# Optimization experiments

Hardware: AMD Instinct MI355X
Metric: run time of the kernel (lower is better)

The kernel has to match this reference:

```python
import jax, jax.numpy as jnp
import numpy as np

B, N, D, V, K = 64, 256, 512, 50257, 100
NORM_TERM = float(np.log(V))        # norm_term='auto' -> log(vocab)
BACKOFF_PROB = 1e-10


def setup_inputs() -> dict:
    key = jax.random.key(0)
    k1, k2, k3, k4, k5 = jax.random.split(key, 5)
    inp = jax.random.normal(k1, (B, N, D), jnp.float32)
    emb_weight = jax.random.normal(k2, (V, D), jnp.float32) * 0.02
    emb_bias = jnp.zeros((V,), jnp.float32)
    # noise distribution buffer: probs clamped + renormed, then log (as in __init__)
    freqs = jax.random.uniform(k3, (V,), jnp.float32, 1e-3, 1.0)
    probs = freqs / freqs.sum()
    probs = jnp.clip(probs, BACKOFF_PROB)
    logprob_noise = jnp.log(probs / probs.sum())
    target = jax.random.randint(k4, (B, N), 0, V)
    # alias.draw(1,1,K).expand(B,N,K): a single shared set of K noise samples
    noise_samples = jax.random.randint(k5, (K,), 0, V)
    return {
        "input": inp,
        "emb_weight": emb_weight,
        "emb_bias": emb_bias,
        "logprob_noise": logprob_noise,
        "target": target,
        "noise_samples": noise_samples,
    }


def reference(input, emb_weight, emb_bias, logprob_noise, target, noise_samples):
    k = noise_samples.shape[0]
    # logits under the noise distribution (pure gathers)
    logit_target_in_noise = logprob_noise[target]          # (B, N)
    logit_noise_in_noise = logprob_noise[noise_samples]    # (K,)
    # model scores: gathered embedding rows dotted with hidden states
    tgt_emb = emb_weight[target]                           # (B, N, D)
    logit_target_in_model = (
        jnp.einsum("bnd,bnd->bn", input, tgt_emb) + emb_bias[target] - NORM_TERM
    )                                                      # (B, N)
    noise_emb = emb_weight[noise_samples]                  # (K, D)
    logit_noise_in_model = (
        jnp.einsum("bnd,kd->bnk", input, noise_emb)
        + emb_bias[noise_samples][None, None, :]
        - NORM_TERM
    )                                                      # (B, N, K)
    # NCE: p_true = exp(lm) / (exp(lm) + K*exp(ln)) = sigmoid(lm - ln - log K)
    # BCE with label [1, 0, ..., 0]:
    #   -loss = log_sigmoid(x) at target slot, log_sigmoid(-x) at noise slots
    log_k = jnp.log(jnp.asarray(k, dtype=input.dtype))
    x_t = logit_target_in_model - logit_target_in_noise - log_k             # (B, N)
    x_n = logit_noise_in_model - logit_noise_in_noise[None, None, :] - log_k  # (B, N, K)
    per_pos = jax.nn.log_sigmoid(x_t) + jnp.sum(jax.nn.log_sigmoid(-x_n), axis=2)
    return jnp.sum(per_pos, axis=1)  # (B,)
```

## Files before the change

kernel.cpp:

```cpp
#include <hip/hip_runtime.h>
#include <math.h>

#define Dq 512
#define Vq 50257
#define Kq 100
#define KP 112
#define NORM_TERM 10.8249051f
#define LOGK 4.6051702f
#define NBLK 512
#define DT_STRIDE 3584

typedef __attribute__((ext_vector_type(8))) short short8;
typedef __attribute__((ext_vector_type(4))) float floatx4;
typedef __attribute__((ext_vector_type(4))) unsigned short ushort4v;
typedef __attribute__((ext_vector_type(8))) unsigned short ushort8v;

__device__ __forceinline__ unsigned short f2bf(float f) {
    union { float f; unsigned u; } v; v.f = f;
    unsigned r = v.u + 0x7FFFu + ((v.u >> 16) & 1u);
    return (unsigned short)(r >> 16);
}

__device__ __forceinline__ short8 cvt8(floatx4 a, floatx4 b) {
    short8 o;
    o[0] = (short)f2bf(a.x); o[1] = (short)f2bf(a.y);
    o[2] = (short)f2bf(a.z); o[3] = (short)f2bf(a.w);
    o[4] = (short)f2bf(b.x); o[5] = (short)f2bf(b.y);
    o[6] = (short)f2bf(b.z); o[7] = (short)f2bf(b.w);
    return o;
}

__device__ __forceinline__ float dot4(floatx4 a, floatx4 b) {
    return a.x*b.x + a.y*b.y + a.z*b.z + a.w*b.w;
}

__device__ __forceinline__ float log_sigmoid(float x) {
    return fminf(x, 0.f) - __logf(1.f + __expf(-fabsf(x)));
}

__global__ void prep_noise(const float* __restrict__ emb_w,
                           const float* __restrict__ emb_b,
                           const float* __restrict__ lpn,
                           const int* __restrict__ ns,
                           unsigned short* __restrict__ nBT,
                           float* __restrict__ nAdj,
                           float* __restrict__ out) {
    int k = blockIdx.x;
    int t = threadIdx.x;
    size_t off = (size_t)(t >> 3) * DT_STRIDE + k * 32 + (t & 7) * 4;
    if (k < Kq) {
        int row = ns[k];
        floatx4 v = ((const floatx4*)(emb_w + (size_t)row * Dq))[t];
        ushort4v o;
        o.x = f2bf(v.x); o.y = f2bf(v.y); o.z = f2bf(v.z); o.w = f2bf(v.w);
        *(ushort4v*)(nBT + off) = o;
        if (t == 0) nAdj[k] = emb_b[row] - NORM_TERM - lpn[row] - LOGK;
    } else {
        ushort4v z; z.x = 0; z.y = 0; z.z = 0; z.w = 0;
        *(ushort4v*)(nBT + off) = z;
        if (t == 0) nAdj[k] = 0.f;
    }
    if (k == 0 && t < 64) out[t] = 0.f;
}

__global__ __launch_bounds__(512, 4) void nce_main(
    const float* __restrict__ input,
    const float* __restrict__ emb_w,
    const float* __restrict__ emb_b,
    const float* __restrict__ lpn,
    const int* __restrict__ target,
    const unsigned short* __restrict__ nBT,
    const float* __restrict__ nAdj,
    float* __restrict__ out)
{
    __shared__ unsigned short A_lds[32 * 512];
    __shared__ float tdot[32];
    __shared__ float blocksum[8];

    int tid  = threadIdx.x;
    int lane = tid & 63;
    int w    = tid >> 6;
    int pos0 = (int)blockIdx.x * 32;
    int r16  = lane & 15;
    int g4   = lane >> 4;

#pragma unroll
    for (int j = 0; j < 4; ++j) {
        int row = w * 4 + j;
        const float* src = input + (size_t)(pos0 + row) * Dq + lane * 8;
        int tg = target[pos0 + row];
        const float* tsrc = emb_w + (size_t)tg * Dq + lane * 8;
        floatx4 x0 = *(const floatx4*)(src);
        floatx4 x1 = *(const floatx4*)(src + 4);
        floatx4 t0 = *(const floatx4*)(tsrc);
        floatx4 t1 = *(const floatx4*)(tsrc + 4);
        float s = dot4(x0, t0) + dot4(x1, t1);
#pragma unroll
        for (int off = 32; off >= 1; off >>= 1)
            s += __shfl_xor(s, off);
        if (lane == 0) tdot[row] = s;
        char* base = (char*)A_lds + row * 1024;
        *(ushort8v*)(base + ((lane * 16) ^ ((row & 7) << 4))) = (ushort8v)cvt8(x0, x1);
    }
    __syncthreads();

    float contrib = 0.f;

    if (w < 7) {
        const char* a0base = (const char*)A_lds + r16 * 1024;
        const char* a1base = a0base + 16 * 1024;
        int asw = (r16 & 7) << 4;
        const unsigned short* p = nBT + (size_t)w * 512 + r16 * 32 + g4 * 8;
        floatx4 acc0 = {0.f, 0.f, 0.f, 0.f};
        floatx4 acc1 = {0.f, 0.f, 0.f, 0.f};
#pragma unroll
        for (int dt = 0; dt < 16; ++dt) {
            int aoff = (dt * 64 + g4 * 16) ^ asw;
            short8 a0 = *(const short8*)(a0base + aoff);
            short8 a1 = *(const short8*)(a1base + aoff);
            short8 f  = *(const short8*)(p + (size_t)dt * DT_STRIDE);
            acc0 = __builtin_amdgcn_mfma_f32_16x16x32_bf16(a0, f, acc0, 0, 0, 0);
            acc1 = __builtin_amdgcn_mfma_f32_16x16x32_bf16(a1, f, acc1, 0, 0, 0);
        }
        int k = w * 16 + r16;
        if (k < Kq) {
            float adj = nAdj[k];
#pragma unroll
            for (int r = 0; r < 4; ++r) {
                contrib += log_sigmoid(-(acc0[r] + adj));
                contrib += log_sigmoid(-(acc1[r] + adj));
            }
        }
    } else {
        if (g4 < 2) {
            int p32 = g4 * 16 + r16;
            int tg = target[pos0 + p32];
            float xt = tdot[p32] + emb_b[tg] - NORM_TERM - lpn[tg] - LOGK;
            contrib += log_sigmoid(xt);
        }
    }

#pragma unroll
    for (int off = 32; off >= 1; off >>= 1)
        contrib += __shfl_xor(contrib, off);
    if (lane == 0) blocksum[w] = contrib;
    __syncthreads();

    if (tid == 0) {
        float s = 0.f;
#pragma unroll
        for (int i = 0; i < 8; ++i) s += blocksum[i];
        atomicAdd(&out[blockIdx.x >> 3], s);
    }
}

extern "C" void kernel_launch(void* const* d_in, const int* in_sizes, int n_in,
                              void* d_out, int out_size, void* d_ws, size_t ws_size,
                              hipStream_t stream) {
    const float* input = (const float*)d_in[0];
    const float* emb_w = (const float*)d_in[1];
    const float* emb_b = (const float*)d_in[2];
    const float* lpn   = (const float*)d_in[3];
    const int*   tgt   = (const int*)d_in[4];
    const int*   ns    = (const int*)d_in[5];
    float* out = (float*)d_out;

    unsigned short* nBT = (unsigned short*)d_ws;
    float* nAdj         = (float*)((char*)d_ws + (size_t)KP * Dq * 2);

    prep_noise<<<KP, 128, 0, stream>>>(emb_w, emb_b, lpn, ns, nBT, nAdj, out);
    nce_main<<<NBLK, 512, 0, stream>>>(input, emb_w, emb_b, lpn, tgt,
                                       nBT, nAdj, out);
}
```

Before: 27.23 us.

## Split each 32-position block into two blocks dividing noise tiles

```diff
diff --git a/kernel.cpp b/kernel.cpp
--- a/kernel.cpp
+++ b/kernel.cpp
@@ -7,7 +7,7 @@
 #define KP 112
 #define NORM_TERM 10.8249051f
 #define LOGK 4.6051702f
-#define NBLK 512
+#define NBLK 1024
 #define DT_STRIDE 3584
 
 typedef __attribute__((ext_vector_type(8))) short short8;
@@ -80,7 +80,8 @@
     int tid  = threadIdx.x;
     int lane = tid & 63;
     int w    = tid >> 6;
-    int pos0 = (int)blockIdx.x * 32;
+    int h    = (int)blockIdx.x & 1;
+    int pos0 = ((int)blockIdx.x >> 1) * 32;
     int r16  = lane & 15;
     int g4   = lane >> 4;
 
@@ -88,52 +89,50 @@
     for (int j = 0; j < 4; ++j) {
         int row = w * 4 + j;
         const float* src = input + (size_t)(pos0 + row) * Dq + lane * 8;
-        int tg = target[pos0 + row];
-        const float* tsrc = emb_w + (size_t)tg * Dq + lane * 8;
         floatx4 x0 = *(const floatx4*)(src);
         floatx4 x1 = *(const floatx4*)(src + 4);
-        floatx4 t0 = *(const floatx4*)(tsrc);
-        floatx4 t1 = *(const floatx4*)(tsrc + 4);
-        float s = dot4(x0, t0) + dot4(x1, t1);
+        if (h) {
+            int tg = target[pos0 + row];
+            const float* tsrc = emb_w + (size_t)tg * Dq + lane * 8;
+            floatx4 t0 = *(const floatx4*)(tsrc);
+            floatx4 t1 = *(const floatx4*)(tsrc + 4);
+            float s = dot4(x0, t0) + dot4(x1, t1);
 #pragma unroll
-        for (int off = 32; off >= 1; off >>= 1)
-            s += __shfl_xor(s, off);
-        if (lane == 0) tdot[row] = s;
+            for (int off = 32; off >= 1; off >>= 1)
+                s += __shfl_xor(s, off);
+            if (lane == 0) tdot[row] = s;
+        }
         char* base = (char*)A_lds + row * 1024;
         *(ushort8v*)(base + ((lane * 16) ^ ((row & 7) << 4))) = (ushort8v)cvt8(x0, x1);
     }
     __syncthreads();
 
     float contrib = 0.f;
+    int w4 = w & 3;
+    int rh = w >> 2;
 
-    if (w < 7) {
-        const char* a0base = (const char*)A_lds + r16 * 1024;
-        const char* a1base = a0base + 16 * 1024;
+    if (h == 0 || w4 < 3) {
+        int kt = h * 4 + w4;
+        const char* abase = (const char*)A_lds + (rh * 16 + r16) * 1024;
         int asw = (r16 & 7) << 4;
-        const unsigned short* p = nBT + (size_t)w * 512 + r16 * 32 + g4 * 8;
-        floatx4 acc0 = {0.f, 0.f, 0.f, 0.f};
-        floatx4 acc1 = {0.f, 0.f, 0.f, 0.f};
+        const unsigned short* p = nBT + (size_t)kt * 512 + r16 * 32 + g4 * 8;
+        floatx4 acc = {0.f, 0.f, 0.f, 0.f};
 #pragma unroll
         for (int dt = 0; dt < 16; ++dt) {
-            int aoff = (dt * 64 + g4 * 16) ^ asw;
-            short8 a0 = *(const short8*)(a0base + aoff);
-            short8 a1 = *(const short8*)(a1base + aoff);
-            short8 f  = *(const short8*)(p + (size_t)dt * DT_STRIDE);
-            acc0 = __builtin_amdgcn_mfma_f32_16x16x32_bf16(a0, f, acc0, 0, 0, 0);
-            acc1 = __builtin_amdgcn_mfma_f32_16x16x32_bf16(a1, f, acc1, 0, 0, 0);
+            short8 a = *(const short8*)(abase + ((dt * 64 + g4 * 16) ^ asw));
+            short8 f = *(const short8*)(p + (size_t)dt * DT_STRIDE);
+            acc = __builtin_amdgcn_mfma_f32_16x16x32_bf16(a, f, acc, 0, 0, 0);
         }
-        int k = w * 16 + r16;
+        int k = kt * 16 + r16;
         if (k < Kq) {
             float adj = nAdj[k];
 #pragma unroll
-            for (int r = 0; r < 4; ++r) {
-                contrib += log_sigmoid(-(acc0[r] + adj));
-                contrib += log_sigmoid(-(acc1[r] + adj));
-            }
+            for (int r = 0; r < 4; ++r)
+                contrib += log_sigmoid(-(acc[r] + adj));
         }
     } else {
-        if (g4 < 2) {
-            int p32 = g4 * 16 + r16;
+        if (g4 == 0) {
+            int p32 = rh * 16 + r16;
             int tg = target[pos0 + p32];
             float xt = tdot[p32] + emb_b[tg] - NORM_TERM - lpn[tg] - LOGK;
             contrib += log_sigmoid(xt);
@@ -150,7 +149,7 @@
         float s = 0.f;
 #pragma unroll
         for (int i = 0; i < 8; ++i) s += blocksum[i];
-        atomicAdd(&out[blockIdx.x >> 3], s);
+        atomicAdd(&out[blockIdx.x >> 4], s);
     }
 }
 
```

Measured after the change: 32.47 us. 19.3% more time.

## Overlap second-half input staging with MFMA on first 16 rows

Applied to the files above, without the earlier changes.

```diff
diff --git a/kernel.cpp b/kernel.cpp
--- a/kernel.cpp
+++ b/kernel.cpp
@@ -85,8 +85,8 @@
     int g4   = lane >> 4;
 
 #pragma unroll
-    for (int j = 0; j < 4; ++j) {
-        int row = w * 4 + j;
+    for (int j = 0; j < 2; ++j) {
+        int row = w * 2 + j;
         const float* src = input + (size_t)(pos0 + row) * Dq + lane * 8;
         int tg = target[pos0 + row];
         const float* tsrc = emb_w + (size_t)tg * Dq + lane * 8;
@@ -104,23 +104,49 @@
     }
     __syncthreads();
 
+    const char* a0base = (const char*)A_lds + r16 * 1024;
+    const char* a1base = a0base + 16 * 1024;
+    int asw = (r16 & 7) << 4;
+    const unsigned short* p = nBT + (size_t)w * 512 + r16 * 32 + g4 * 8;
+    floatx4 acc0 = {0.f, 0.f, 0.f, 0.f};
+    floatx4 acc1 = {0.f, 0.f, 0.f, 0.f};
+
+#pragma unroll
+    for (int ph = 0; ph < 2; ++ph) {
+        int row = 16 + ph * 8 + w;
+        const float* src = input + (size_t)(pos0 + row) * Dq + lane * 8;
+        int tg = target[pos0 + row];
+        const float* tsrc = emb_w + (size_t)tg * Dq + lane * 8;
+        floatx4 x0 = *(const floatx4*)(src);
+        floatx4 x1 = *(const floatx4*)(src + 4);
+        floatx4 t0 = *(const floatx4*)(tsrc);
+        floatx4 t1 = *(const floatx4*)(tsrc + 4);
+        if (w < 7) {
+#pragma unroll
+            for (int d = 0; d < 8; ++d) {
+                int dt = ph * 8 + d;
+                short8 a = *(const short8*)(a0base + ((dt * 64 + g4 * 16) ^ asw));
+                short8 f = *(const short8*)(p + (size_t)dt * DT_STRIDE);
+                acc0 = __builtin_amdgcn_mfma_f32_16x16x32_bf16(a, f, acc0, 0, 0, 0);
+            }
+        }
+        float s = dot4(x0, t0) + dot4(x1, t1);
+#pragma unroll
+        for (int off = 32; off >= 1; off >>= 1)
+            s += __shfl_xor(s, off);
+        if (lane == 0) tdot[row] = s;
+        char* base = (char*)A_lds + row * 1024;
+        *(ushort8v*)(base + ((lane * 16) ^ ((row & 7) << 4))) = (ushort8v)cvt8(x0, x1);
+    }
+    __syncthreads();
+
     float contrib = 0.f;
-
     if (w < 7) {
-        const char* a0base = (const char*)A_lds + r16 * 1024;
-        const char* a1base = a0base + 16 * 1024;
-        int asw = (r16 & 7) << 4;
-        const unsigned short* p = nBT + (size_t)w * 512 + r16 * 32 + g4 * 8;
-        floatx4 acc0 = {0.f, 0.f, 0.f, 0.f};
-        floatx4 acc1 = {0.f, 0.f, 0.f, 0.f};
 #pragma unroll
         for (int dt = 0; dt < 16; ++dt) {
-            int aoff = (dt * 64 + g4 * 16) ^ asw;
-            short8 a0 = *(const short8*)(a0base + aoff);
-            short8 a1 = *(const short8*)(a1base + aoff);
-            short8 f  = *(const short8*)(p + (size_t)dt * DT_STRIDE);
-            acc0 = __builtin_amdgcn_mfma_f32_16x16x32_bf16(a0, f, acc0, 0, 0, 0);
-            acc1 = __builtin_amdgcn_mfma_f32_16x16x32_bf16(a1, f, acc1, 0, 0, 0);
+            short8 a = *(const short8*)(a1base + ((dt * 64 + g4 * 16) ^ asw));
+            short8 f = *(const short8*)(p + (size_t)dt * DT_STRIDE);
+            acc1 = __builtin_amdgcn_mfma_f32_16x16x32_bf16(a, f, acc1, 0, 0, 0);
         }
         int k = w * 16 + r16;
         if (k < Kq) {
```

After: 27.35 us. No clear change (+0.5%).
